# Optimization experiments

Measured on AMD Instinct MI355X. Metric: run time of the kernel, lower is better.

## Reference

```python
import jax, jax.numpy as jnp
import numpy as np


def _lstm_cell(gates, c_prev):
    # PyTorch gate order: input, forget, cell(g), output
    i, f, g, o = jnp.split(gates, 4, axis=-1)
    c = jax.nn.sigmoid(f) * c_prev + jax.nn.sigmoid(i) * jnp.tanh(g)
    h = jax.nn.sigmoid(o) * jnp.tanh(c)
    return h, c


def setup_inputs() -> dict:
    key = jax.random.key(0)
    ks = jax.random.split(key, 20)
    s = 0.1
    x = jax.random.normal(ks[0], (1, 1, 37), dtype=jnp.float32)
    # active flags live at columns 12 + 5*opp_id; set opponents 0,2,3 active (==1)
    act_idx = 12 + 5 * jnp.arange(5)
    flags = jnp.array([1.0, 0.0, 1.0, 1.0, 0.0], dtype=jnp.float32)
    x = x.at[0, 0, act_idx].set(flags)
    inp = {
        'x': x,
        'gen_Wih': s * jax.random.normal(ks[1], (10, 40, 12), dtype=jnp.float32),
        'gen_Whh': s * jax.random.normal(ks[2], (10, 40, 10), dtype=jnp.float32),
        'gen_bih': s * jax.random.normal(ks[3], (10, 40), dtype=jnp.float32),
        'gen_bhh': s * jax.random.normal(ks[4], (10, 40), dtype=jnp.float32),
        'gen_h0': s * jax.random.normal(ks[5], (10, 10), dtype=jnp.float32),
        'gen_c0': s * jax.random.normal(ks[6], (10, 10), dtype=jnp.float32),
        'game_Wih': s * jax.random.normal(ks[7], (5, 10, 20, 4), dtype=jnp.float32),
        'game_Whh': s * jax.random.normal(ks[8], (5, 10, 20, 5), dtype=jnp.float32),
        'game_bih': s * jax.random.normal(ks[9], (5, 10, 20), dtype=jnp.float32),
        'game_bhh': s * jax.random.normal(ks[10], (5, 10, 20), dtype=jnp.float32),
        'game_h0': s * jax.random.normal(ks[11], (5, 10, 5), dtype=jnp.float32),
        'game_c0': s * jax.random.normal(ks[12], (5, 10, 5), dtype=jnp.float32),
        'W1': s * jax.random.normal(ks[13], (50, 200), dtype=jnp.float32),
        'b1': s * jax.random.normal(ks[14], (50,), dtype=jnp.float32),
        'W2': s * jax.random.normal(ks[15], (10, 50), dtype=jnp.float32),
        'b2': s * jax.random.normal(ks[16], (10,), dtype=jnp.float32),
        'W3': s * jax.random.normal(ks[17], (1, 10), dtype=jnp.float32),
        'b3': s * jax.random.normal(ks[18], (1,), dtype=jnp.float32),
    }
    return inp


def reference(x, gen_Wih, gen_Whh, gen_bih, gen_bhh, gen_h0, gen_c0,
              game_Wih, game_Whh, game_bih, game_bhh, game_h0, game_c0,
              W1, b1, W2, b2, W3, b3):
    # seq_len = batch = 1 (forced by the view(1,1,-1) -> Linear(200) shapes)
    xg = x[0, 0, :12]                                     # [12] general features
    # 10 independent LSTM(12,10) cells, batched via einsum over the cell axis k
    gates_g = (jnp.einsum('kgd,d->kg', gen_Wih, xg)
               + jnp.einsum('kgh,kh->kg', gen_Whh, gen_h0)
               + gen_bih + gen_bhh)                       # [10, 40]
    h_gen, _ = _lstm_cell(gates_g, gen_c0)                # [10, 10]
    x_gen_out = h_gen.reshape(-1)                         # [100]

    xo = x[0, 0, 12:37].reshape(5, 5)                     # 5 opponents x 5 feats
    active = xo[:, 0]                                     # active flag
    feats = xo[:, 1:]                                     # [5, 4]
    # 5 opponents x 10 independent LSTM(4,5) game cells
    gates_o = (jnp.einsum('okgd,od->okg', game_Wih, feats)
               + jnp.einsum('okgh,okh->okg', game_Whh, game_h0)
               + game_bih + game_bhh)                     # [5, 10, 20]
    h_game, _ = _lstm_cell(gates_o, game_c0)              # [5, 10, 5]
    game_flat = h_game.reshape(5, 50)
    # Bug replicated from source: the round loop concatenates x_opp_game (the
    # stale output of game-LSTM #9) 10 times; round LSTM outputs are unused.
    repeated = jnp.tile(h_game[:, 9, :], (1, 10))         # [5, 50]
    opp_single = jnp.concatenate([game_flat, repeated], axis=1)  # [5, 100]

    mask = (active == 1.0).astype(x.dtype)                # 'if x_active == 1'
    opp_avg = (mask[:, None] * opp_single).sum(0) / mask.sum()   # mean over active

    test = jnp.concatenate([x_gen_out, opp_avg])          # [200]
    h1 = jnp.tanh(test @ W1.T + b1)
    h2 = jnp.tanh(h1 @ W2.T + b2)
    out = jnp.tanh(h2 @ W3.T + b3)
    return out.reshape(1, 1, 1)
```

## Files before the change

kernel.cpp:

```cpp
#include <hip/hip_runtime.h>
#include <math.h>


__device__ __forceinline__ float sigf(float v) {
    return 1.0f / (1.0f + expf(-v));
}

__global__ __launch_bounds__(256) void net6max_kernel(
    const float* __restrict__ x,
    const float* __restrict__ gen_Wih,
    const float* __restrict__ gen_Whh,
    const float* __restrict__ gen_bih,
    const float* __restrict__ gen_bhh,
    const float* __restrict__ gen_h0,
    const float* __restrict__ gen_c0,
    const float* __restrict__ game_Wih,
    const float* __restrict__ game_Whh,
    const float* __restrict__ game_bih,
    const float* __restrict__ game_bhh,
    const float* __restrict__ game_h0,
    const float* __restrict__ game_c0,
    const float* __restrict__ W1,
    const float* __restrict__ b1,
    const float* __restrict__ W2,
    const float* __restrict__ b2,
    const float* __restrict__ W3,
    const float* __restrict__ b3,
    float* __restrict__ out)
{
    __shared__ float s_xg[12];
    __shared__ float s_feats[5][4];
    __shared__ float s_active[5];
    __shared__ float s_gates_g[10][40];
    __shared__ float s_gates_o[5][10][20];
    __shared__ float s_hgame[5][10][5];
    __shared__ float s_test[200];
    __shared__ float s_h1[50];
    __shared__ float s_h2[10];

    const int tid = threadIdx.x;

    if (tid < 12) s_xg[tid] = x[tid];
    if (tid >= 32 && tid < 32 + 25) {
        int j = tid - 32;
        int o = j / 5, c = j % 5;
        float v = x[12 + j];
        if (c == 0) s_active[o] = v;
        else        s_feats[o][c - 1] = v;
    }
    __syncthreads();

    for (int idx = tid; idx < 400; idx += 256) {
        int k = idx / 40, g = idx % 40;
        const float* wih = gen_Wih + (size_t)(k * 40 + g) * 12;
        const float* whh = gen_Whh + (size_t)(k * 40 + g) * 10;
        const float* h0  = gen_h0 + k * 10;
        float acc = gen_bih[idx] + gen_bhh[idx];
        #pragma unroll
        for (int d = 0; d < 12; ++d) acc += wih[d] * s_xg[d];
        #pragma unroll
        for (int h = 0; h < 10; ++h) acc += whh[h] * h0[h];
        s_gates_g[k][g] = acc;
    }

    for (int idx = tid; idx < 1000; idx += 256) {
        int o = idx / 200;
        int rem = idx % 200;
        int k = rem / 20, g = rem % 20;
        const float* wih = game_Wih + (size_t)((o * 10 + k) * 20 + g) * 4;
        const float* whh = game_Whh + (size_t)((o * 10 + k) * 20 + g) * 5;
        const float* h0  = game_h0 + (o * 10 + k) * 5;
        float acc = game_bih[idx] + game_bhh[idx];
        #pragma unroll
        for (int d = 0; d < 4; ++d) acc += wih[d] * s_feats[o][d];
        #pragma unroll
        for (int h = 0; h < 5; ++h) acc += whh[h] * h0[h];
        s_gates_o[o][k][g] = acc;
    }
    __syncthreads();

    if (tid < 100) {
        int k = tid / 10, j = tid % 10;
        float gi = s_gates_g[k][j];
        float gf = s_gates_g[k][10 + j];
        float gg = s_gates_g[k][20 + j];
        float go = s_gates_g[k][30 + j];
        float c = sigf(gf) * gen_c0[k * 10 + j] + sigf(gi) * tanhf(gg);
        s_test[tid] = sigf(go) * tanhf(c);
    }
    if (tid < 250) {
        int o = tid / 50;
        int rem = tid % 50;
        int k = rem / 5, j = rem % 5;
        float gi = s_gates_o[o][k][j];
        float gf = s_gates_o[o][k][5 + j];
        float gg = s_gates_o[o][k][10 + j];
        float go = s_gates_o[o][k][15 + j];
        float c = sigf(gf) * game_c0[(o * 10 + k) * 5 + j] + sigf(gi) * tanhf(gg);
        s_hgame[o][k][j] = sigf(go) * tanhf(c);
    }
    __syncthreads();

    if (tid < 100) {
        float msum = 0.0f, acc = 0.0f;
        #pragma unroll
        for (int o = 0; o < 5; ++o) {
            float m = (s_active[o] == 1.0f) ? 1.0f : 0.0f;
            msum += m;
            float v = (tid < 50) ? s_hgame[o][tid / 5][tid % 5]
                                 : s_hgame[o][9][(tid - 50) % 5];
            acc += m * v;
        }
        s_test[100 + tid] = acc / msum;
    }
    __syncthreads();

    if (tid < 50) {
        const float* w = W1 + (size_t)tid * 200;
        float acc = b1[tid];
        for (int c = 0; c < 200; ++c) acc += w[c] * s_test[c];
        s_h1[tid] = tanhf(acc);
    }
    __syncthreads();

    if (tid < 10) {
        const float* w = W2 + (size_t)tid * 50;
        float acc = b2[tid];
        #pragma unroll
        for (int c = 0; c < 50; ++c) acc += w[c] * s_h1[c];
        s_h2[tid] = tanhf(acc);
    }
    __syncthreads();

    if (tid == 0) {
        float acc = b3[0];
        #pragma unroll
        for (int c = 0; c < 10; ++c) acc += W3[c] * s_h2[c];
        out[0] = tanhf(acc);
    }
}

extern "C" void kernel_launch(void* const* d_in, const int* in_sizes, int n_in,
                              void* d_out, int out_size, void* d_ws, size_t ws_size,
                              hipStream_t stream) {
    (void)in_sizes; (void)n_in; (void)out_size; (void)d_ws; (void)ws_size;
    const float* x        = (const float*)d_in[0];
    const float* gen_Wih  = (const float*)d_in[1];
    const float* gen_Whh  = (const float*)d_in[2];
    const float* gen_bih  = (const float*)d_in[3];
    const float* gen_bhh  = (const float*)d_in[4];
    const float* gen_h0   = (const float*)d_in[5];
    const float* gen_c0   = (const float*)d_in[6];
    const float* game_Wih = (const float*)d_in[7];
    const float* game_Whh = (const float*)d_in[8];
    const float* game_bih = (const float*)d_in[9];
    const float* game_bhh = (const float*)d_in[10];
    const float* game_h0  = (const float*)d_in[11];
    const float* game_c0  = (const float*)d_in[12];
    const float* W1       = (const float*)d_in[13];
    const float* b1       = (const float*)d_in[14];
    const float* W2       = (const float*)d_in[15];
    const float* b2       = (const float*)d_in[16];
    const float* W3       = (const float*)d_in[17];
    const float* b3       = (const float*)d_in[18];
    float* out = (float*)d_out;

    net6max_kernel<<<1, 256, 0, stream>>>(
        x, gen_Wih, gen_Whh, gen_bih, gen_bhh, gen_h0, gen_c0,
        game_Wih, game_Whh, game_bih, game_bhh, game_h0, game_c0,
        W1, b1, W2, b2, W3, b3, out);
}
```

Before: 11.23 us.

## Widen block to 1024 threads, vectorize gate loads, use fast math intrinsics

Launches 1024 threads so every gate pre-activation gets its own thread instead of looping. Weight and activation loads become float4/float2 vector loads. The W1 and W2 dot products are split across 4 and 2 lanes and combined with shuffles. sigmoid and tanh now use __expf/__fdividef approximations. These target the latency of a single small block, at the cost of slightly different numerics and reliance on vector alignment of the input buffers.

Result: faster. 10.71 us, median of 2 (-4.6%).

```diff
diff --git a/kernel.cpp b/kernel.cpp
--- a/kernel.cpp
+++ b/kernel.cpp
@@ -2,11 +2,14 @@
 #include <math.h>
 
 
-__device__ __forceinline__ float sigf(float v) {
-    return 1.0f / (1.0f + expf(-v));
-}
-
-__global__ __launch_bounds__(256) void net6max_kernel(
+__device__ __forceinline__ float fsig(float v) {
+    return __fdividef(1.0f, 1.0f + __expf(-v));
+}
+__device__ __forceinline__ float ftanh(float v) {
+    return 1.0f - __fdividef(2.0f, 1.0f + __expf(2.0f * v));
+}
+
+__global__ __launch_bounds__(1024) void net6max_kernel(
     const float* __restrict__ x,
     const float* __restrict__ gen_Wih,
     const float* __restrict__ gen_Whh,
@@ -28,21 +31,21 @@
     const float* __restrict__ b3,
     float* __restrict__ out)
 {
-    __shared__ float s_xg[12];
-    __shared__ float s_feats[5][4];
-    __shared__ float s_active[5];
-    __shared__ float s_gates_g[10][40];
-    __shared__ float s_gates_o[5][10][20];
-    __shared__ float s_hgame[5][10][5];
-    __shared__ float s_test[200];
-    __shared__ float s_h1[50];
-    __shared__ float s_h2[10];
+    __shared__ __align__(16) float s_xg[12];
+    __shared__ __align__(16) float s_feats[5][4];
+    __shared__ __align__(16) float s_active[8];
+    __shared__ __align__(16) float s_gates_g[400];
+    __shared__ __align__(16) float s_gates_o[1000];
+    __shared__ __align__(16) float s_hgame[5][10][5];
+    __shared__ __align__(16) float s_test[200];
+    __shared__ __align__(16) float s_h1[52];
+    __shared__ __align__(16) float s_h2[12];
 
     const int tid = threadIdx.x;
 
     if (tid < 12) s_xg[tid] = x[tid];
-    if (tid >= 32 && tid < 32 + 25) {
-        int j = tid - 32;
+    if (tid >= 64 && tid < 64 + 25) {
+        int j = tid - 64;
         int o = j / 5, c = j % 5;
         float v = x[12 + j];
         if (c == 0) s_active[o] = v;
@@ -50,54 +53,63 @@
     }
     __syncthreads();
 
-    for (int idx = tid; idx < 400; idx += 256) {
-        int k = idx / 40, g = idx % 40;
-        const float* wih = gen_Wih + (size_t)(k * 40 + g) * 12;
-        const float* whh = gen_Whh + (size_t)(k * 40 + g) * 10;
-        const float* h0  = gen_h0 + k * 10;
-        float acc = gen_bih[idx] + gen_bhh[idx];
-        #pragma unroll
-        for (int d = 0; d < 12; ++d) acc += wih[d] * s_xg[d];
-        #pragma unroll
-        for (int h = 0; h < 10; ++h) acc += whh[h] * h0[h];
-        s_gates_g[k][g] = acc;
-    }
-
-    for (int idx = tid; idx < 1000; idx += 256) {
-        int o = idx / 200;
-        int rem = idx % 200;
-        int k = rem / 20, g = rem % 20;
-        const float* wih = game_Wih + (size_t)((o * 10 + k) * 20 + g) * 4;
-        const float* whh = game_Whh + (size_t)((o * 10 + k) * 20 + g) * 5;
-        const float* h0  = game_h0 + (o * 10 + k) * 5;
-        float acc = game_bih[idx] + game_bhh[idx];
-        #pragma unroll
-        for (int d = 0; d < 4; ++d) acc += wih[d] * s_feats[o][d];
-        #pragma unroll
-        for (int h = 0; h < 5; ++h) acc += whh[h] * h0[h];
-        s_gates_o[o][k][g] = acc;
+    if (tid < 400) {
+        int k = tid / 40;
+        const float4* wih4 = (const float4*)(gen_Wih + (size_t)tid * 12);
+        const float2* whh2 = (const float2*)(gen_Whh + (size_t)tid * 10);
+        const float2* h02  = (const float2*)(gen_h0 + k * 10);
+        float4 xa = *(const float4*)&s_xg[0];
+        float4 xb = *(const float4*)&s_xg[4];
+        float4 xc = *(const float4*)&s_xg[8];
+        float4 p4 = wih4[0] * xa + wih4[1] * xb + wih4[2] * xc;
+        float2 q2 = whh2[0] * h02[0] + whh2[1] * h02[1] + whh2[2] * h02[2]
+                  + whh2[3] * h02[3] + whh2[4] * h02[4];
+        float acc = gen_bih[tid] + gen_bhh[tid]
+                  + p4.x + p4.y + p4.z + p4.w + q2.x + q2.y;
+        s_gates_g[tid] = acc;
+    }
+
+    {
+        int gt = -1;
+        if (tid < 400)       gt = 600 + tid;
+        else if (tid >= 424) gt = tid - 424;
+        if (gt >= 0) {
+            int o   = gt / 200;
+            int ok_ = gt / 20;
+            const float4* wih4 = (const float4*)(game_Wih + (size_t)gt * 4);
+            const float*  whh  = game_Whh + (size_t)gt * 5;
+            const float*  h0   = game_h0 + ok_ * 5;
+            float4 f4 = *(const float4*)&s_feats[o][0];
+            float4 p  = wih4[0] * f4;
+            float acc = game_bih[gt] + game_bhh[gt] + p.x + p.y + p.z + p.w;
+            acc += whh[0]*h0[0] + whh[1]*h0[1] + whh[2]*h0[2]
+                 + whh[3]*h0[3] + whh[4]*h0[4];
+            s_gates_o[gt] = acc;
+        }
     }
     __syncthreads();
 
     if (tid < 100) {
         int k = tid / 10, j = tid % 10;
-        float gi = s_gates_g[k][j];
-        float gf = s_gates_g[k][10 + j];
-        float gg = s_gates_g[k][20 + j];
-        float go = s_gates_g[k][30 + j];
-        float c = sigf(gf) * gen_c0[k * 10 + j] + sigf(gi) * tanhf(gg);
-        s_test[tid] = sigf(go) * tanhf(c);
-    }
-    if (tid < 250) {
-        int o = tid / 50;
-        int rem = tid % 50;
+        int base = k * 40;
+        float gi = s_gates_g[base + j];
+        float gf = s_gates_g[base + 10 + j];
+        float gg = s_gates_g[base + 20 + j];
+        float go = s_gates_g[base + 30 + j];
+        float c = fsig(gf) * gen_c0[tid] + fsig(gi) * ftanh(gg);
+        s_test[tid] = fsig(go) * ftanh(c);
+    } else if (tid >= 512 && tid < 512 + 250) {
+        int t = tid - 512;
+        int o = t / 50;
+        int rem = t % 50;
         int k = rem / 5, j = rem % 5;
-        float gi = s_gates_o[o][k][j];
-        float gf = s_gates_o[o][k][5 + j];
-        float gg = s_gates_o[o][k][10 + j];
-        float go = s_gates_o[o][k][15 + j];
-        float c = sigf(gf) * game_c0[(o * 10 + k) * 5 + j] + sigf(gi) * tanhf(gg);
-        s_hgame[o][k][j] = sigf(go) * tanhf(c);
+        int base = (o * 10 + k) * 20;
+        float gi = s_gates_o[base + j];
+        float gf = s_gates_o[base + 5 + j];
+        float gg = s_gates_o[base + 10 + j];
+        float go = s_gates_o[base + 15 + j];
+        float c = fsig(gf) * game_c0[(o * 10 + k) * 5 + j] + fsig(gi) * ftanh(gg);
+        s_hgame[o][k][j] = fsig(go) * ftanh(c);
     }
     __syncthreads();
 
@@ -111,24 +123,45 @@
                                  : s_hgame[o][9][(tid - 50) % 5];
             acc += m * v;
         }
-        s_test[100 + tid] = acc / msum;
-    }
-    __syncthreads();
-
-    if (tid < 50) {
-        const float* w = W1 + (size_t)tid * 200;
-        float acc = b1[tid];
-        for (int c = 0; c < 200; ++c) acc += w[c] * s_test[c];
-        s_h1[tid] = tanhf(acc);
-    }
-    __syncthreads();
-
-    if (tid < 10) {
-        const float* w = W2 + (size_t)tid * 50;
-        float acc = b2[tid];
-        #pragma unroll
-        for (int c = 0; c < 50; ++c) acc += w[c] * s_h1[c];
-        s_h2[tid] = tanhf(acc);
+        s_test[100 + tid] = __fdividef(acc, msum);
+    }
+    __syncthreads();
+
+    if (tid < 200) {
+        int r = tid >> 2, q = tid & 3;
+        const float4* w4 = (const float4*)(W1 + (size_t)r * 200);
+        const float4* t4 = (const float4*)s_test;
+        float4 acc4 = make_float4(0.f, 0.f, 0.f, 0.f);
+        #pragma unroll
+        for (int m = 0; m < 12; ++m) {
+            int c4 = q + 4 * m;
+            acc4 += w4[c4] * t4[c4];
+        }
+        if (q < 2) {
+            int c4 = 48 + q;
+            acc4 += w4[c4] * t4[c4];
+        }
+        float acc = acc4.x + acc4.y + acc4.z + acc4.w;
+        acc += __shfl_xor(acc, 1);
+        acc += __shfl_xor(acc, 2);
+        if (q == 0) s_h1[r] = ftanh(acc + b1[r]);
+    }
+    __syncthreads();
+
+    if (tid < 20) {
+        int r = tid >> 1, q = tid & 1;
+        const float2* w2 = (const float2*)(W2 + (size_t)r * 50);
+        const float2* h2 = (const float2*)s_h1;
+        float2 acc2 = make_float2(0.f, 0.f);
+        #pragma unroll
+        for (int m = 0; m < 12; ++m) {
+            int c = q + 2 * m;
+            acc2 += w2[c] * h2[c];
+        }
+        if (q == 0) acc2 += w2[24] * h2[24];
+        float acc = acc2.x + acc2.y;
+        acc += __shfl_xor(acc, 1);
+        if (q == 0) s_h2[r] = ftanh(acc + b2[r]);
     }
     __syncthreads();
 
@@ -136,7 +169,7 @@
         float acc = b3[0];
         #pragma unroll
         for (int c = 0; c < 10; ++c) acc += W3[c] * s_h2[c];
-        out[0] = tanhf(acc);
+        out[0] = ftanh(acc);
     }
 }
 
@@ -165,7 +198,7 @@
     const float* b3       = (const float*)d_in[18];
     float* out = (float*)d_out;
 
-    net6max_kernel<<<1, 256, 0, stream>>>(
+    net6max_kernel<<<1, 1024, 0, stream>>>(
         x, gen_Wih, gen_Whh, gen_bih, gen_bhh, gen_h0, gen_c0,
         game_Wih, game_Whh, game_bih, game_bhh, game_h0, game_c0,
         W1, b1, W2, b2, W3, b3, out);
```
